# Kernel tuning notes

Measured on AMD Instinct MI355X. Metric: run time of the kernel, lower is better.

## Reference

```python
import jax, jax.numpy as jnp
import numpy as np

N = 4096  # flattened_input_shape


def setup_inputs() -> dict:
    key = jax.random.key(0)
    ks = jax.random.split(key, 5)
    eps = 0.1
    center = jax.random.normal(ks[0], (1, N), dtype=jnp.float32)
    lb0 = center - eps  # initial interval lower bounds [1, N]
    ub0 = center + eps  # initial interval upper bounds [1, N]
    W1 = jax.random.normal(ks[1], (N, N), dtype=jnp.float32) / np.float32(np.sqrt(N))
    b1 = jax.random.normal(ks[2], (1, N), dtype=jnp.float32)
    W2 = jax.random.normal(ks[3], (N, N), dtype=jnp.float32) / np.float32(np.sqrt(N))
    b2 = jax.random.normal(ks[4], (1, N), dtype=jnp.float32)
    raw_alpha = jnp.ones((N,), dtype=jnp.float32)  # nn.Parameter init
    return {"raw_alpha": raw_alpha, "lb0": lb0, "ub0": ub0,
            "W1": W1, "b1": b1, "W2": W2, "b2": b2}


def _pos(x):
    return jnp.where(x > 0, x, jnp.zeros_like(x))


def _neg(x):
    return jnp.where(x < 0, x, jnp.zeros_like(x))


def _forward(raw_alpha, lb0, ub0, W1, b1, W2, b2):
    # ---- previous.backsubstitution(): compose affine2 over affine1 ----
    clslope, clintercept = W2, b2
    cuslope, cuintercept = W2, b2
    clp, cln = _pos(clslope), _neg(clslope)
    cup, cun = _pos(cuslope), _neg(cuslope)
    clintercept = b1 @ clp.T + b1 @ cln.T + clintercept  # [1, N]
    cuintercept = b1 @ cup.T + b1 @ cun.T + cuintercept  # [1, N]
    clslope = clp @ W1 + cln @ W1  # [N, N]
    cuslope = cup @ W1 + cun @ W1  # [N, N]
    # ---- certifier against initial interval bounds ----
    lbounds = lb0 @ _pos(clslope).T + ub0 @ _neg(clslope).T + clintercept  # [1, N]
    ubounds = ub0 @ _pos(cuslope).T + lb0 @ _neg(cuslope).T + cuintercept  # [1, N]
    # ---- DeepPolyReLU transformer ----
    alpha = jax.nn.sigmoid(raw_alpha)  # [N]
    lb = lbounds.reshape(-1)
    ub = ubounds.reshape(-1)
    denom = ub - lb
    # ub/(ub-lb) with NaN (0/0) replaced by 0, grad-safe
    relu_slope = jnp.where(denom == 0, 0.0, ub / jnp.where(denom == 0, 1.0, denom))  # [N]
    relu_intercept = (1.0 - relu_slope)[None, :] * ubounds  # [1, N]
    below = ub <= 0
    above = lb >= 0
    crossing = ~(below | above)
    base = jnp.where(above, 1.0, 0.0)  # [N]
    uslope = jnp.where(crossing, relu_slope, base)
    uintercept = jnp.where(crossing[None, :], relu_intercept, jnp.zeros((1, N), dtype=ubounds.dtype))
    lslope_v1 = jnp.where(crossing, 0.0, base)
    lslope_v2 = jnp.where(crossing, 1.0, base)
    lslope = alpha * lslope_v1 + (1.0 - alpha) * lslope_v2  # [N]
    lintercept = jnp.zeros((1, N), dtype=lbounds.dtype)
    return jnp.diag(lslope), lintercept, jnp.diag(uslope), uintercept


def reference(raw_alpha, lb0, ub0, W1, b1, W2, b2):
    return _forward(raw_alpha, lb0, ub0, W1, b1, W2, b2)
```

## Files before the change

### kernel.cpp

```cpp
#include <hip/hip_runtime.h>
#include <stdint.h>

#define N 4096

#define TILE_BYTES 524288
#define KT_BYTES   16384

#define QSCALE 256.0f
#define INV_QQ (1.0f / 65536.0f)

typedef int v8i __attribute__((ext_vector_type(8)));
typedef float f32x16 __attribute__((ext_vector_type(16)));

union V8 { v8i v; uint4 h[2]; };

__device__ __forceinline__ void gload16(const unsigned char* g, unsigned char* l) {
  __builtin_amdgcn_global_load_lds(
      (const __attribute__((address_space(1))) unsigned int*)g,
      (__attribute__((address_space(3))) unsigned int*)l, 16, 0, 0);
}

__device__ __forceinline__ int pack4_fp8(float a, float b, float c, float d) {
  int r = __builtin_amdgcn_cvt_pk_fp8_f32(a, b, 0, false);
  r = __builtin_amdgcn_cvt_pk_fp8_f32(c, d, r, true);
  return r;
}

__global__ __launch_bounds__(256) void prep_w1(const float* __restrict__ W1,
                                               const float* __restrict__ lb0,
                                               const float* __restrict__ ub0,
                                               unsigned char* __restrict__ W1T,
                                               float* __restrict__ tvec) {
  __shared__ float tile[64 * 65];
  __shared__ float tdot[64];
  const int t = threadIdx.x;
  const int j0 = blockIdx.x * 64, k0 = blockIdx.y * 64;
#pragma unroll
  for (int s = 0; s < 4; ++s) {
    int ck = s * 256 + t;
    int row = ck >> 4;
    int col = (ck & 15) * 4;
    float4 v = *(const float4*)(W1 + (size_t)(k0 + row) * N + j0 + col);
    float4 l = *(const float4*)(lb0 + j0 + col);
    float4 u = *(const float4*)(ub0 + j0 + col);
    float part = v.x * 0.5f * (l.x + u.x) + v.y * 0.5f * (l.y + u.y)
               + v.z * 0.5f * (l.z + u.z) + v.w * 0.5f * (l.w + u.w);
    part += __shfl_xor(part, 1, 64);
    part += __shfl_xor(part, 2, 64);
    part += __shfl_xor(part, 4, 64);
    part += __shfl_xor(part, 8, 64);
    if ((t & 15) == 0) tdot[row] = part;
    float* d = &tile[row * 65 + col];
    d[0] = v.x; d[1] = v.y; d[2] = v.z; d[3] = v.w;
  }
  __syncthreads();
  if (t < 64) atomicAdd(&tvec[k0 + t], tdot[t]);
  int jl = t >> 2, ch = (t & 3) * 16;
  float f[16];
#pragma unroll
  for (int m = 0; m < 16; ++m) f[m] = tile[(ch + m) * 65 + jl] * QSCALE;
  uint4 o;
  o.x = (unsigned)pack4_fp8(f[0], f[1], f[2], f[3]);
  o.y = (unsigned)pack4_fp8(f[4], f[5], f[6], f[7]);
  o.z = (unsigned)pack4_fp8(f[8], f[9], f[10], f[11]);
  o.w = (unsigned)pack4_fp8(f[12], f[13], f[14], f[15]);
  int j = j0 + jl;
  int kb = k0 + ch;
  *(uint4*)(W1T + (size_t)(j >> 7) * TILE_BYTES + (size_t)(kb >> 7) * KT_BYTES
            + (size_t)((kb >> 4) & 7) * 2048 + (j & 127) * 16) = o;
}

__global__ __launch_bounds__(256) void convert_w2(const float* __restrict__ W2,
                                                  const float* __restrict__ b1,
                                                  const float* __restrict__ tvec,
                                                  unsigned char* __restrict__ W2q,
                                                  float* __restrict__ cvec,
                                                  float* __restrict__ Sc) {
  const int t = threadIdx.x;
  const int i0 = blockIdx.y * 128;
  const int k0 = blockIdx.x * 128;
  const int r = t & 127;
  const int h = t >> 7;
  unsigned char* panel = W2q + (size_t)blockIdx.y * TILE_BYTES
                       + (size_t)blockIdx.x * KT_BYTES;
  float dotb = 0.f, dott = 0.f;
#pragma unroll
  for (int q = 0; q < 4; ++q) {
    int c = 2 * q + h;
    const float* p = W2 + (size_t)(i0 + r) * N + k0 + c * 16;
    alignas(16) int packed[4];
#pragma unroll
    for (int m = 0; m < 4; ++m) {
      float4 w = *(const float4*)(p + m * 4);
      float4 b = *(const float4*)(b1 + k0 + c * 16 + m * 4);
      float4 tv = *(const float4*)(tvec + k0 + c * 16 + m * 4);
      dotb += w.x * b.x + w.y * b.y + w.z * b.z + w.w * b.w;
      dott += w.x * tv.x + w.y * tv.y + w.z * tv.z + w.w * tv.w;
      packed[m] = pack4_fp8(w.x * QSCALE, w.y * QSCALE, w.z * QSCALE, w.w * QSCALE);
    }
    *(uint4*)(panel + (size_t)c * 2048 + r * 16) = *(const uint4*)packed;
  }
  __shared__ float redb[256], redt[256];
  redb[t] = dotb;
  redt[t] = dott;
  __syncthreads();
  if (t < 128) {
    float vb = redb[t] + redb[t + 128];
    float vt = redt[t] + redt[t + 128];
    atomicAdd(&cvec[i0 + t], vb);
    atomicAdd(&Sc[i0 + t], vt);
  }
}

#define NT 32
__global__ __launch_bounds__(512, 2) void gemm_absrow(const unsigned char* __restrict__ A,
                                                      const unsigned char* __restrict__ B,
                                                      const float* __restrict__ lb0,
                                                      const float* __restrict__ ub0,
                                                      float* __restrict__ R_acc) {
  __shared__ __align__(16) unsigned char sm[4 * 32768];
  const int t = threadIdx.x;
  const int lane = t & 63, w = t >> 6;
  const int wr = w >> 2, wc = w & 3;
  const int l31 = lane & 31, half = lane >> 5;

  const int bid = blockIdx.y * 16 + blockIdx.x;
  const int swz = (bid & 7) * 32 + (bid >> 3);
  const int bm = swz >> 4, bn = swz & 15;
  const int i0 = bm * 256, j0 = bn * 256;

  const unsigned char* gA0 = A + (size_t)(2 * bm) * TILE_BYTES + t * 16;
  const unsigned char* gA1 = gA0 + TILE_BYTES;
  const unsigned char* gB0 = B + (size_t)(2 * bn) * TILE_BYTES + t * 16;
  const unsigned char* gB1 = gB0 + TILE_BYTES;

  f32x16 acc[4][2] = {};
  const int sc1 = 0x7F7F7F7F;

  auto stage = [&](int kt, int h) {
    const int g = ((kt & 1) << 1) | h;
    unsigned char* d = sm + g * 32768 + t * 16;
    const size_t off = (size_t)kt * KT_BYTES + (size_t)h * 8192;
    gload16(gA0 + off, d);
    gload16(gA1 + off, d + 8192);
    gload16(gB0 + off, d + 16384);
    gload16(gB1 + off, d + 24576);
  };

  auto compute = [&](int kt, int h) {
    const unsigned char* base = sm + (((kt & 1) << 1) | h) * 32768;
    V8 af[4], bf[2];
    const unsigned char* pa = base + wr * 8192 + (half * 2) * 2048 + l31 * 16;
#pragma unroll
    for (int tm = 0; tm < 4; ++tm) {
      const unsigned char* p = pa + tm * 512;
      af[tm].h[0] = *(const uint4*)p;
      af[tm].h[1] = *(const uint4*)(p + 2048);
    }
#pragma unroll
    for (int tn = 0; tn < 2; ++tn) {
      const int j = wc * 64 + tn * 32 + l31;
      const unsigned char* p = base + 16384 + (j >> 7) * 8192
                             + (half * 2) * 2048 + (j & 127) * 16;
      bf[tn].h[0] = *(const uint4*)p;
      bf[tn].h[1] = *(const uint4*)(p + 2048);
    }
    __builtin_amdgcn_s_setprio(1);
#pragma unroll
    for (int tm = 0; tm < 4; ++tm)
#pragma unroll
      for (int tn = 0; tn < 2; ++tn)
        acc[tm][tn] = __builtin_amdgcn_mfma_scale_f32_32x32x64_f8f6f4(
            af[tm].v, bf[tn].v, acc[tm][tn],
            0 , 0 ,
            0, sc1, 0, sc1);
    __builtin_amdgcn_s_setprio(0);
  };

  stage(0, 0);
  stage(0, 1);

  for (int kt = 0; kt < NT - 1; ++kt) {
#pragma unroll
    for (int h = 0; h < 2; ++h) {
      stage(kt + 1, h);
      asm volatile("s_waitcnt vmcnt(8)" ::: "memory");
      __builtin_amdgcn_s_barrier();
      asm volatile("" ::: "memory");
      compute(kt, h);
    }
  }
  asm volatile("s_waitcnt vmcnt(4)" ::: "memory");
  __builtin_amdgcn_s_barrier();
  asm volatile("" ::: "memory");
  compute(NT - 1, 0);
  asm volatile("s_waitcnt vmcnt(0)" ::: "memory");
  __builtin_amdgcn_s_barrier();
  asm volatile("" ::: "memory");
  compute(NT - 1, 1);

  float epsv[2];
#pragma unroll
  for (int tn = 0; tn < 2; ++tn) {
    int j = j0 + wc * 64 + tn * 32 + l31;
    epsv[tn] = 0.5f * (ub0[j] - lb0[j]);
  }
#pragma unroll
  for (int tm = 0; tm < 4; ++tm) {
#pragma unroll
    for (int r = 0; r < 16; ++r) {
      float s = fabsf(acc[tm][0][r]) * epsv[0] + fabsf(acc[tm][1][r]) * epsv[1];
#pragma unroll
      for (int off = 1; off < 32; off <<= 1)
        s += __shfl_xor(s, off, 64);
      if (l31 == 0) {
        int i = i0 + wr * 128 + tm * 32 + (r & 3) + 8 * (r >> 2) + 4 * half;
        atomicAdd(&R_acc[i], s);
      }
    }
  }
}

struct ReluVals { float lslope, uslope, uinter; };

__device__ __forceinline__ ReluVals relu_vals(int i,
                                              const float* __restrict__ cvec,
                                              const float* __restrict__ Sc,
                                              const float* __restrict__ b2,
                                              const float* __restrict__ R_acc,
                                              const float* __restrict__ raw_alpha) {
  float mid = Sc[i] + cvec[i] + b2[i];
  float rr = R_acc[i] * INV_QQ;
  float lb = mid - rr;
  float ub = mid + rr;
  float alpha = 1.f / (1.f + expf(-raw_alpha[i]));
  float denom = ub - lb;
  float slope = (denom == 0.f) ? 0.f : ub / denom;
  bool below = ub <= 0.f, above = lb >= 0.f;
  bool crossing = !(below || above);
  float base = above ? 1.f : 0.f;
  ReluVals v;
  v.uslope = crossing ? slope : base;
  v.uinter = crossing ? (1.f - slope) * ub : 0.f;
  float l1 = crossing ? 0.f : base;
  float l2 = crossing ? 1.f : base;
  v.lslope = alpha * l1 + (1.f - alpha) * l2;
  return v;
}

__global__ __launch_bounds__(256) void fill_patch(float4* __restrict__ out, int n4,
                                                  const float* __restrict__ cvec,
                                                  const float* __restrict__ Sc,
                                                  const float* __restrict__ b2,
                                                  const float* __restrict__ R_acc,
                                                  const float* __restrict__ raw_alpha) {
  const size_t NN = (size_t)N * N;
  const size_t d1_end = NN;
  const size_t d2_beg = NN + N;
  const size_t d2_end = 2 * NN + N;
  int idx = blockIdx.x * 256 + threadIdx.x;
  int stride = gridDim.x * 256;
  for (int i = idx; i < n4; i += stride) {
    size_t e = 4 * (size_t)i;
    float4 v = make_float4(0.f, 0.f, 0.f, 0.f);
    if (e >= d2_end) {
      int b = (int)(e - d2_end);
      v.x = relu_vals(b + 0, cvec, Sc, b2, R_acc, raw_alpha).uinter;
      v.y = relu_vals(b + 1, cvec, Sc, b2, R_acc, raw_alpha).uinter;
      v.z = relu_vals(b + 2, cvec, Sc, b2, R_acc, raw_alpha).uinter;
      v.w = relu_vals(b + 3, cvec, Sc, b2, R_acc, raw_alpha).uinter;
    } else if (e < d1_end) {
      int r = (int)(e >> 12), c = (int)(e & 4095);
      if (r >= c && r < c + 4)
        (&v.x)[r - c] = relu_vals(r, cvec, Sc, b2, R_acc, raw_alpha).lslope;
    } else if (e >= d2_beg) {
      size_t e2 = e - d2_beg;
      int r = (int)(e2 >> 12), c = (int)(e2 & 4095);
      if (r >= c && r < c + 4)
        (&v.x)[r - c] = relu_vals(r, cvec, Sc, b2, R_acc, raw_alpha).uslope;
    }
    out[i] = v;
  }
}

extern "C" void kernel_launch(void* const* d_in, const int* in_sizes, int n_in,
                              void* d_out, int out_size, void* d_ws, size_t ws_size,
                              hipStream_t stream) {
  const float* raw_alpha = (const float*)d_in[0];
  const float* lb0 = (const float*)d_in[1];
  const float* ub0 = (const float*)d_in[2];
  const float* W1 = (const float*)d_in[3];
  const float* b1 = (const float*)d_in[4];
  const float* W2 = (const float*)d_in[5];
  const float* b2 = (const float*)d_in[6];

  float* tvec = (float*)d_ws;
  float* cvec = tvec + N;
  float* Sc = cvec + N;
  float* R_acc = Sc + N;

  unsigned char* W2q = (unsigned char*)d_out;
  unsigned char* W1Tq = W2q + (size_t)N * N;

  (void)hipMemsetAsync(d_ws, 0, 4 * N * sizeof(float), stream);
  prep_w1<<<dim3(N / 64, N / 64), 256, 0, stream>>>(W1, lb0, ub0, W1Tq, tvec);
  convert_w2<<<dim3(N / 128, N / 128), 256, 0, stream>>>(W2, b1, tvec, W2q, cvec, Sc);
  gemm_absrow<<<dim3(16, 16), 512, 0, stream>>>(W2q, W1Tq, lb0, ub0, R_acc);
  int n4 = out_size / 4;
  fill_patch<<<8192, 256, 0, stream>>>((float4*)d_out, n4, cvec, Sc, b2, R_acc, raw_alpha);
}
```

Before: 357.2 us.

## Deepen GEMM LDS pipeline, coalesce W2 conversion, use nontemporal output stores

The fp8 GEMM loop now keeps three half-k stages in flight across four LDS buffers instead of two. LDS fragment reads use inline ds_read_b128 with immediate offsets, issued before the next global-to-LDS prefetch and before the barrier, so they can overlap. convert_w2 now reads W2 rows coalesced and reduces them with warp shuffles, then transposes the packed fp8 through shared memory before writing panels. The final output store is made nontemporal. The inline asm and manual vmcnt counts are brittle, and the extra barrier per phase adds synchronisation.

Measured after the change: 354.5 us. Within noise of the previous version (-0.7%).

```diff
diff --git a/kernel.cpp b/kernel.cpp
--- a/kernel.cpp
+++ b/kernel.cpp
@@ -11,8 +11,10 @@
 
 typedef int v8i __attribute__((ext_vector_type(8)));
 typedef float f32x16 __attribute__((ext_vector_type(16)));
-
-union V8 { v8i v; uint4 h[2]; };
+typedef unsigned int u32x4 __attribute__((ext_vector_type(4)));
+typedef float f32x4 __attribute__((ext_vector_type(4)));
+
+union V8 { v8i v; u32x4 h[2]; };
 
 __device__ __forceinline__ void gload16(const unsigned char* g, unsigned char* l) {
   __builtin_amdgcn_global_load_lds(
@@ -76,43 +78,52 @@
                                                   unsigned char* __restrict__ W2q,
                                                   float* __restrict__ cvec,
                                                   float* __restrict__ Sc) {
+  __shared__ int lpack[128][33];
   const int t = threadIdx.x;
   const int i0 = blockIdx.y * 128;
   const int k0 = blockIdx.x * 128;
-  const int r = t & 127;
-  const int h = t >> 7;
+  const int kl = (t & 31) * 4;
+  const int rsub = t >> 5;
+  float4 bv = *(const float4*)(b1 + k0 + kl);
+  float4 tv = *(const float4*)(tvec + k0 + kl);
+#pragma unroll
+  for (int s = 0; s < 16; ++s) {
+    int row = s * 8 + rsub;
+    float4 w = *(const float4*)(W2 + (size_t)(i0 + row) * N + k0 + kl);
+    float db = w.x * bv.x + w.y * bv.y + w.z * bv.z + w.w * bv.w;
+    float dt = w.x * tv.x + w.y * tv.y + w.z * tv.z + w.w * tv.w;
+    db += __shfl_xor(db, 1, 64);  dt += __shfl_xor(dt, 1, 64);
+    db += __shfl_xor(db, 2, 64);  dt += __shfl_xor(dt, 2, 64);
+    db += __shfl_xor(db, 4, 64);  dt += __shfl_xor(dt, 4, 64);
+    db += __shfl_xor(db, 8, 64);  dt += __shfl_xor(dt, 8, 64);
+    db += __shfl_xor(db, 16, 64); dt += __shfl_xor(dt, 16, 64);
+    if ((t & 31) == 0) {
+      atomicAdd(&cvec[i0 + row], db);
+      atomicAdd(&Sc[i0 + row], dt);
+    }
+    lpack[row][t & 31] = pack4_fp8(w.x * QSCALE, w.y * QSCALE,
+                                   w.z * QSCALE, w.w * QSCALE);
+  }
+  __syncthreads();
   unsigned char* panel = W2q + (size_t)blockIdx.y * TILE_BYTES
                        + (size_t)blockIdx.x * KT_BYTES;
-  float dotb = 0.f, dott = 0.f;
 #pragma unroll
   for (int q = 0; q < 4; ++q) {
-    int c = 2 * q + h;
-    const float* p = W2 + (size_t)(i0 + r) * N + k0 + c * 16;
-    alignas(16) int packed[4];
-#pragma unroll
-    for (int m = 0; m < 4; ++m) {
-      float4 w = *(const float4*)(p + m * 4);
-      float4 b = *(const float4*)(b1 + k0 + c * 16 + m * 4);
-      float4 tv = *(const float4*)(tvec + k0 + c * 16 + m * 4);
-      dotb += w.x * b.x + w.y * b.y + w.z * b.z + w.w * b.w;
-      dott += w.x * tv.x + w.y * tv.y + w.z * tv.z + w.w * tv.w;
-      packed[m] = pack4_fp8(w.x * QSCALE, w.y * QSCALE, w.z * QSCALE, w.w * QSCALE);
-    }
-    *(uint4*)(panel + (size_t)c * 2048 + r * 16) = *(const uint4*)packed;
-  }
-  __shared__ float redb[256], redt[256];
-  redb[t] = dotb;
-  redt[t] = dott;
-  __syncthreads();
-  if (t < 128) {
-    float vb = redb[t] + redb[t + 128];
-    float vt = redt[t] + redt[t + 128];
-    atomicAdd(&cvec[i0 + t], vb);
-    atomicAdd(&Sc[i0 + t], vt);
+    int cid = q * 256 + t;
+    int r = cid & 127, c = cid >> 7;
+    uint4 o;
+    o.x = (unsigned)lpack[r][4 * c + 0];
+    o.y = (unsigned)lpack[r][4 * c + 1];
+    o.z = (unsigned)lpack[r][4 * c + 2];
+    o.w = (unsigned)lpack[r][4 * c + 3];
+    *(uint4*)(panel + (size_t)c * 2048 + r * 16) = o;
   }
 }
 
 #define NT 32
+#define DSR(dst, addr, OFF) \
+  asm volatile("ds_read_b128 %0, %1 offset:" OFF : "=v"(dst) : "v"(addr))
+
 __global__ __launch_bounds__(512, 2) void gemm_absrow(const unsigned char* __restrict__ A,
                                                       const unsigned char* __restrict__ B,
                                                       const float* __restrict__ lb0,
@@ -137,67 +148,70 @@
   f32x16 acc[4][2] = {};
   const int sc1 = 0x7F7F7F7F;
 
-  auto stage = [&](int kt, int h) {
-    const int g = ((kt & 1) << 1) | h;
-    unsigned char* d = sm + g * 32768 + t * 16;
-    const size_t off = (size_t)kt * KT_BYTES + (size_t)h * 8192;
+  const unsigned lds0 =
+      (unsigned)(size_t)(__attribute__((address_space(3))) unsigned char*)sm;
+  const unsigned aoff = lds0 + wr * 8192 + half * 4096 + l31 * 16;
+  const int jb0 = wc * 64 + l31, jb1 = jb0 + 32;
+  const unsigned boff0 = lds0 + 16384 + (jb0 >> 7) * 8192 + half * 4096 + (jb0 & 127) * 16;
+  const unsigned boff1 = lds0 + 16384 + (jb1 >> 7) * 8192 + half * 4096 + (jb1 & 127) * 16;
+
+  auto stage = [&](int g) {
+    unsigned char* d = sm + (size_t)(g & 3) * 32768 + t * 16;
+    const size_t off = (size_t)(g >> 1) * KT_BYTES + (size_t)(g & 1) * 8192;
     gload16(gA0 + off, d);
     gload16(gA1 + off, d + 8192);
     gload16(gB0 + off, d + 16384);
     gload16(gB1 + off, d + 24576);
   };
 
-  auto compute = [&](int kt, int h) {
-    const unsigned char* base = sm + (((kt & 1) << 1) | h) * 32768;
-    V8 af[4], bf[2];
-    const unsigned char* pa = base + wr * 8192 + (half * 2) * 2048 + l31 * 16;
-#pragma unroll
-    for (int tm = 0; tm < 4; ++tm) {
-      const unsigned char* p = pa + tm * 512;
-      af[tm].h[0] = *(const uint4*)p;
-      af[tm].h[1] = *(const uint4*)(p + 2048);
-    }
-#pragma unroll
-    for (int tn = 0; tn < 2; ++tn) {
-      const int j = wc * 64 + tn * 32 + l31;
-      const unsigned char* p = base + 16384 + (j >> 7) * 8192
-                             + (half * 2) * 2048 + (j & 127) * 16;
-      bf[tn].h[0] = *(const uint4*)p;
-      bf[tn].h[1] = *(const uint4*)(p + 2048);
-    }
-    __builtin_amdgcn_s_setprio(1);
-#pragma unroll
-    for (int tm = 0; tm < 4; ++tm)
-#pragma unroll
-      for (int tn = 0; tn < 2; ++tn)
-        acc[tm][tn] = __builtin_amdgcn_mfma_scale_f32_32x32x64_f8f6f4(
-            af[tm].v, bf[tn].v, acc[tm][tn],
-            0 , 0 ,
-            0, sc1, 0, sc1);
-    __builtin_amdgcn_s_setprio(0);
-  };
-
-  stage(0, 0);
-  stage(0, 1);
-
-  for (int kt = 0; kt < NT - 1; ++kt) {
-#pragma unroll
-    for (int h = 0; h < 2; ++h) {
-      stage(kt + 1, h);
-      asm volatile("s_waitcnt vmcnt(8)" ::: "memory");
-      __builtin_amdgcn_s_barrier();
-      asm volatile("" ::: "memory");
-      compute(kt, h);
-    }
-  }
+  V8 af[4], bf[2];
+
+#define PHASE_LOAD(g)                                                     \
+  {                                                                       \
+    unsigned sb = (unsigned)((g) & 3) * 32768u;                           \
+    unsigned sa = aoff + sb, s0 = boff0 + sb, s1 = boff1 + sb;            \
+    DSR(af[0].h[0], sa, "0");    DSR(af[0].h[1], sa, "2048");             \
+    DSR(af[1].h[0], sa, "512");  DSR(af[1].h[1], sa, "2560");             \
+    DSR(af[2].h[0], sa, "1024"); DSR(af[2].h[1], sa, "3072");             \
+    DSR(af[3].h[0], sa, "1536"); DSR(af[3].h[1], sa, "3584");             \
+    DSR(bf[0].h[0], s0, "0");    DSR(bf[0].h[1], s0, "2048");             \
+    DSR(bf[1].h[0], s1, "0");    DSR(bf[1].h[1], s1, "2048");             \
+  }
+
+#define PHASE_MFMA()                                                      \
+  asm volatile("s_waitcnt lgkmcnt(0)" ::: "memory");                      \
+  __builtin_amdgcn_sched_barrier(0);                                      \
+  __builtin_amdgcn_s_setprio(1);                                          \
+  _Pragma("unroll") for (int tm = 0; tm < 4; ++tm)                        \
+    _Pragma("unroll") for (int tn = 0; tn < 2; ++tn)                      \
+      acc[tm][tn] = __builtin_amdgcn_mfma_scale_f32_32x32x64_f8f6f4(      \
+          af[tm].v, bf[tn].v, acc[tm][tn], 0, 0, 0, sc1, 0, sc1);         \
+  __builtin_amdgcn_s_setprio(0);
+
+  stage(0); stage(1); stage(2);
+  asm volatile("s_waitcnt vmcnt(8)" ::: "memory");
+  __builtin_amdgcn_s_barrier();
+
+  for (int g = 0; g < 61; ++g) {
+    PHASE_LOAD(g);
+    stage(g + 3);
+    asm volatile("s_waitcnt vmcnt(8)" ::: "memory");
+    __builtin_amdgcn_s_barrier();
+    PHASE_MFMA();
+    __builtin_amdgcn_s_barrier();
+  }
+  PHASE_LOAD(61);
   asm volatile("s_waitcnt vmcnt(4)" ::: "memory");
   __builtin_amdgcn_s_barrier();
-  asm volatile("" ::: "memory");
-  compute(NT - 1, 0);
+  PHASE_MFMA();
+  __builtin_amdgcn_s_barrier();
+  PHASE_LOAD(62);
   asm volatile("s_waitcnt vmcnt(0)" ::: "memory");
   __builtin_amdgcn_s_barrier();
-  asm volatile("" ::: "memory");
-  compute(NT - 1, 1);
+  PHASE_MFMA();
+  __builtin_amdgcn_s_barrier();
+  PHASE_LOAD(63);
+  PHASE_MFMA();
 
   float epsv[2];
 #pragma unroll
@@ -279,7 +293,8 @@
       if (r >= c && r < c + 4)
         (&v.x)[r - c] = relu_vals(r, cvec, Sc, b2, R_acc, raw_alpha).uslope;
     }
-    out[i] = v;
+    f32x4 vv = {v.x, v.y, v.z, v.w};
+    __builtin_nontemporal_store(vv, (f32x4*)(out + i));
   }
 }
 
```
